# Performance work log

Measured on AMD Instinct MI355X. Metric: run time of the kernel, lower is better.

## Reference

```python
import jax, jax.numpy as jnp
import numpy as np

H, W = 256, 256
SIGMA = 1.5
INV_VAR = 1.0 / (2.0 * (SIGMA ** 2 + 1e-08))

def setup_inputs() -> dict:
    key = jax.random.key(0)
    k1, k2 = jax.random.split(key)
    B, K, N = 4, 8, 4096
    # pixel-coordinate points, slightly over-ranged to test edge behavior
    points_2d = jax.random.uniform(k1, (B, K, N, 2), dtype=jnp.float32,
                                   minval=-4.0, maxval=260.0)
    points_z = jax.random.uniform(k2, (B, K, N), dtype=jnp.float32,
                                  minval=0.0, maxval=5.0)
    return {"points_2d": points_2d, "points_z": points_z}

def reference(points_2d, points_z):
    # points_2d: (B, K, N, 2); points_z: (B, K, N)
    x = points_2d[..., 0]                      # (B,K,N)
    y = points_2d[..., 1]                      # (B,K,N)
    xg = jnp.arange(W, dtype=points_2d.dtype)  # (W,)
    yg = jnp.arange(H, dtype=points_2d.dtype)  # (H,)
    # Separable Gaussian: exp(-(dx^2+dy^2)*c) = exp(-dx^2*c) * exp(-dy^2*c)
    wx = jnp.exp(-((xg - x[..., None]) ** 2) * INV_VAR)  # (B,K,N,W)
    wy = jnp.exp(-((yg - y[..., None]) ** 2) * INV_VAR)  # (B,K,N,H)
    inv_z = 1.0 / jnp.clip(points_z, 1e-05, None)        # (B,K,N)
    wy = wy * inv_z[..., None]
    # sum over points of outer products -> (B,K,H,W)
    return jnp.einsum('bknh,bknw->bkhw', wy, wx)
```

## Files before the change

### kernel.cpp

```cpp
#include <hip/hip_runtime.h>
#include <hip/hip_bf16.h>

typedef __attribute__((ext_vector_type(8))) short bf16x8;
typedef __attribute__((ext_vector_type(4))) float f32x4;
typedef __attribute__((ext_vector_type(4))) unsigned int u32x4;

constexpr int NPTS = 4096;
constexpr int HH = 256;
constexpr int WW = 256;
constexpr int PSEG = 256;
constexpr int CCAPW = 288;

#define SCALE_S 0.56621453f
#define DCUT 10.0f

__device__ inline unsigned cvtpk(float lo, float hi) {
    unsigned r;
    asm("v_cvt_pk_bf16_f32 %0, %1, %2" : "=v"(r) : "v"(lo), "v"(hi));
    return r;
}

__global__ __launch_bounds__(256, 2) void soft_raster_kernel(
    const float* __restrict__ p2d,
    const float* __restrict__ pz,
    float* __restrict__ out)
{
    const int bk  = blockIdx.z;
    const int tm  = blockIdx.y * 64;
    const int tn  = blockIdx.x * 64;
    const int tid = threadIdx.x;

    __shared__ __align__(16) float sxs[4 * PSEG], sys[4 * PSEG], szi[4 * PSEG];
    __shared__ __align__(16) float cxs[4 * CCAPW], cys[4 * CCAPW], czi[4 * CCAPW];
    __shared__ int scnt[4];

    const int wid  = tid >> 6;
    const int lane = tid & 63;
    const int tmw  = tm + ((wid >> 1) << 5);
    const int tnw  = tn + ((wid & 1) << 5);
    const int g    = lane >> 4;
    const int r    = lane & 15;

    const size_t pbase = (size_t)bk * NPTS;
    const float4* __restrict__ pxy4 =
        reinterpret_cast<const float4*>(p2d + 2 * pbase);
    const float2* __restrict__ pz2 =
        reinterpret_cast<const float2*>(pz + pbase);

    const float Xlo = (float)tn - DCUT, Xhi = (float)(tn + 63) + DCUT;
    const float Ylo = (float)tm - DCUT, Yhi = (float)(tm + 63) + DCUT;
    const unsigned long long maskl = (1ull << lane) - 1ull;

    float4 P[8];
    float2 Z[8];
    #pragma unroll
    for (int it = 0; it < 8; ++it) P[it] = pxy4[(wid << 9) + (it << 6) + lane];
    #pragma unroll
    for (int it = 0; it < 8; ++it) Z[it] = pz2[(wid << 9) + (it << 6) + lane];

    int base = 0;
    #pragma unroll
    for (int it = 0; it < 8; ++it) {
        const float4 p  = P[it];
        const float2 zz = Z[it];
        bool in0 = (p.x > Xlo) && (p.x < Xhi) && (p.y > Ylo) && (p.y < Yhi);
        bool in1 = (p.z > Xlo) && (p.z < Xhi) && (p.w > Ylo) && (p.w < Yhi);
        unsigned long long be = __ballot(in0);
        unsigned long long bo = __ballot(in1);
        int pos0 = base + __popcll(be & maskl) + __popcll(bo & maskl);
        int pos1 = pos0 + (in0 ? 1 : 0);
        if (in0 && pos0 < PSEG) {
            const int s = (wid << 8) + pos0;
            sxs[s] = p.x * SCALE_S;
            sys[s] = p.y * SCALE_S;
            szi[s] = -__builtin_amdgcn_logf(fmaxf(zz.x, 1e-5f));
        }
        if (in1 && pos1 < PSEG) {
            const int s = (wid << 8) + pos1;
            sxs[s] = p.z * SCALE_S;
            sys[s] = p.w * SCALE_S;
            szi[s] = -__builtin_amdgcn_logf(fmaxf(zz.y, 1e-5f));
        }
        base += __popcll(be) + __popcll(bo);
    }
    if (lane == 0) scnt[wid] = (base < PSEG) ? base : PSEG;
    __syncthreads();

    const float xlo = ((float)tnw - DCUT) * SCALE_S;
    const float xhi = ((float)(tnw + 31) + DCUT) * SCALE_S;
    const float ylo = ((float)tmw - DCUT) * SCALE_S;
    const float yhi = ((float)(tmw + 31) + DCUT) * SCALE_S;
    float* __restrict__ wxs = cxs + wid * CCAPW;
    float* __restrict__ wys = cys + wid * CCAPW;
    float* __restrict__ wzi = czi + wid * CCAPW;

    int cw = 0;
    #pragma unroll
    for (int s = 0; s < 4; ++s) {
        const int cs = scnt[s];
        const int jb = lane << 2;
        const float4 x4 = *reinterpret_cast<const float4*>(&sxs[(s << 8) + jb]);
        const float4 y4 = *reinterpret_cast<const float4*>(&sys[(s << 8) + jb]);
        const float4 z4 = *reinterpret_cast<const float4*>(&szi[(s << 8) + jb]);
        bool i0 = (jb + 0 < cs) && (x4.x > xlo) && (x4.x < xhi) && (y4.x > ylo) && (y4.x < yhi);
        bool i1 = (jb + 1 < cs) && (x4.y > xlo) && (x4.y < xhi) && (y4.y > ylo) && (y4.y < yhi);
        bool i2 = (jb + 2 < cs) && (x4.z > xlo) && (x4.z < xhi) && (y4.z > ylo) && (y4.z < yhi);
        bool i3 = (jb + 3 < cs) && (x4.w > xlo) && (x4.w < xhi) && (y4.w > ylo) && (y4.w < yhi);
        unsigned long long b0 = __ballot(i0), b1 = __ballot(i1);
        unsigned long long b2 = __ballot(i2), b3 = __ballot(i3);
        const int c0 = __popcll(b0), c1 = __popcll(b1), c2 = __popcll(b2);
        int pos0 = cw + __popcll(b0 & maskl);
        int pos1 = cw + c0 + __popcll(b1 & maskl);
        int pos2 = cw + c0 + c1 + __popcll(b2 & maskl);
        int pos3 = cw + c0 + c1 + c2 + __popcll(b3 & maskl);
        if (i0 && pos0 < 256) { wxs[pos0] = x4.x; wys[pos0] = y4.x; wzi[pos0] = z4.x; }
        if (i1 && pos1 < 256) { wxs[pos1] = x4.y; wys[pos1] = y4.y; wzi[pos1] = z4.y; }
        if (i2 && pos2 < 256) { wxs[pos2] = x4.z; wys[pos2] = y4.z; wzi[pos2] = z4.z; }
        if (i3 && pos3 < 256) { wxs[pos3] = x4.w; wys[pos3] = y4.w; wzi[pos3] = z4.w; }
        cw += c0 + c1 + c2 + __popcll(b3);
    }
    cw = (cw < 256) ? cw : 256;
    const int pw = (cw + 31) & ~31;
    for (int j = cw + lane; j < pw; j += 64) {
        wxs[j] = 0.f; wys[j] = 0.f; wzi[j] = -__builtin_inff();
    }

    f32x4 acc[2][2] = {};
    const float qy0 = (float)(tmw + r)      * SCALE_S;
    const float qy1 = (float)(tmw + 16 + r) * SCALE_S;
    const float qx0 = (float)(tnw + r)      * SCALE_S;
    const float qx1 = (float)(tnw + 16 + r) * SCALE_S;

    for (int k0 = 0; k0 < pw; k0 += 32) {
        const int kb = k0 + (g << 3);

        float4 y0 = *reinterpret_cast<const float4*>(&wys[kb]);
        float4 y1 = *reinterpret_cast<const float4*>(&wys[kb + 4]);
        float4 z0 = *reinterpret_cast<const float4*>(&wzi[kb]);
        float4 z1 = *reinterpret_cast<const float4*>(&wzi[kb + 4]);
        float4 x0 = *reinterpret_cast<const float4*>(&wxs[kb]);
        float4 x1 = *reinterpret_cast<const float4*>(&wxs[kb + 4]);

        u32x4 au[2], bu[2];
        #pragma unroll
        for (int mi = 0; mi < 2; ++mi) {
            const float qy = mi ? qy1 : qy0;
            float d;
            d = qy - y0.x; const float a0 = __builtin_amdgcn_exp2f(fmaf(d, -d, z0.x));
            d = qy - y0.y; const float a1 = __builtin_amdgcn_exp2f(fmaf(d, -d, z0.y));
            d = qy - y0.z; const float a2 = __builtin_amdgcn_exp2f(fmaf(d, -d, z0.z));
            d = qy - y0.w; const float a3 = __builtin_amdgcn_exp2f(fmaf(d, -d, z0.w));
            d = qy - y1.x; const float a4 = __builtin_amdgcn_exp2f(fmaf(d, -d, z1.x));
            d = qy - y1.y; const float a5 = __builtin_amdgcn_exp2f(fmaf(d, -d, z1.y));
            d = qy - y1.z; const float a6 = __builtin_amdgcn_exp2f(fmaf(d, -d, z1.z));
            d = qy - y1.w; const float a7 = __builtin_amdgcn_exp2f(fmaf(d, -d, z1.w));
            au[mi][0] = cvtpk(a0, a1); au[mi][1] = cvtpk(a2, a3);
            au[mi][2] = cvtpk(a4, a5); au[mi][3] = cvtpk(a6, a7);
        }
        #pragma unroll
        for (int ni = 0; ni < 2; ++ni) {
            const float qx = ni ? qx1 : qx0;
            float d;
            d = qx - x0.x; const float b0 = __builtin_amdgcn_exp2f(-(d * d));
            d = qx - x0.y; const float b1 = __builtin_amdgcn_exp2f(-(d * d));
            d = qx - x0.z; const float b2 = __builtin_amdgcn_exp2f(-(d * d));
            d = qx - x0.w; const float b3 = __builtin_amdgcn_exp2f(-(d * d));
            d = qx - x1.x; const float b4 = __builtin_amdgcn_exp2f(-(d * d));
            d = qx - x1.y; const float b5 = __builtin_amdgcn_exp2f(-(d * d));
            d = qx - x1.z; const float b6 = __builtin_amdgcn_exp2f(-(d * d));
            d = qx - x1.w; const float b7 = __builtin_amdgcn_exp2f(-(d * d));
            bu[ni][0] = cvtpk(b0, b1); bu[ni][1] = cvtpk(b2, b3);
            bu[ni][2] = cvtpk(b4, b5); bu[ni][3] = cvtpk(b6, b7);
        }
        #pragma unroll
        for (int mi = 0; mi < 2; ++mi)
            #pragma unroll
            for (int ni = 0; ni < 2; ++ni)
                acc[mi][ni] = __builtin_amdgcn_mfma_f32_16x16x32_bf16(
                    __builtin_bit_cast(bf16x8, au[mi]),
                    __builtin_bit_cast(bf16x8, bu[ni]), acc[mi][ni], 0, 0, 0);
    }

    float* obase = out + (size_t)bk * (HH * WW);
    #pragma unroll
    for (int mi = 0; mi < 2; ++mi) {
        #pragma unroll
        for (int ni = 0; ni < 2; ++ni) {
            const int col  = tnw + (ni << 4) + r;
            const int row0 = tmw + (mi << 4) + (g << 2);
            #pragma unroll
            for (int j = 0; j < 4; ++j)
                obase[(size_t)(row0 + j) * WW + col] = acc[mi][ni][j];
        }
    }
}

extern "C" void kernel_launch(void* const* d_in, const int* in_sizes, int n_in,
                              void* d_out, int out_size, void* d_ws, size_t ws_size,
                              hipStream_t stream) {
    const float* p2d = (const float*)d_in[0];
    const float* pz  = (const float*)d_in[1];
    float* out       = (float*)d_out;
    const int nbk    = in_sizes[1] / NPTS;
    dim3 grid(WW / 64, HH / 64, nbk);
    dim3 block(256);
    hipLaunchKernelGGL(soft_raster_kernel, grid, block, 0, stream, p2d, pz, out);
}
```

Baseline: 15.07 us.

## Use 8 waves per block with 16x32 per-wave tiles and smaller candidate caps

Doubles the block to 512 threads (8 waves). Each wave now owns a 16x32 output sub-tile instead of 32x32, and the point-binning load is split across more waves with half the loads per thread. Per-wave candidate lists are capped at 192 points with a tighter y-bounds filter. This is meant to raise parallelism and latency hiding in the exp/MFMA loop. In exchange, the x-direction Gaussian weights are recomputed by twice as many waves, more LDS is used per block, and the lower cap could drop points in dense regions.

After: 17.89 us. +18.7%, slower.

```diff
diff --git a/kernel.cpp b/kernel.cpp
--- a/kernel.cpp
+++ b/kernel.cpp
@@ -8,8 +8,9 @@
 constexpr int NPTS = 4096;
 constexpr int HH = 256;
 constexpr int WW = 256;
-constexpr int PSEG = 256;
-constexpr int CCAPW = 288;
+constexpr int PSEG  = 256;
+constexpr int CWCAP = 192;
+constexpr int CCAPW = 224;
 
 #define SCALE_S 0.56621453f
 #define DCUT 10.0f
@@ -20,7 +21,7 @@
     return r;
 }
 
-__global__ __launch_bounds__(256, 2) void soft_raster_kernel(
+__global__ __launch_bounds__(512, 4) void soft_raster_kernel(
     const float* __restrict__ p2d,
     const float* __restrict__ pz,
     float* __restrict__ out)
@@ -30,13 +31,13 @@
     const int tn  = blockIdx.x * 64;
     const int tid = threadIdx.x;
 
-    __shared__ __align__(16) float sxs[4 * PSEG], sys[4 * PSEG], szi[4 * PSEG];
-    __shared__ __align__(16) float cxs[4 * CCAPW], cys[4 * CCAPW], czi[4 * CCAPW];
-    __shared__ int scnt[4];
+    __shared__ __align__(16) float sxs[8 * PSEG], sys[8 * PSEG], szi[8 * PSEG];
+    __shared__ __align__(16) float cxs[8 * CCAPW], cys[8 * CCAPW], czi[8 * CCAPW];
+    __shared__ int scnt[8];
 
     const int wid  = tid >> 6;
     const int lane = tid & 63;
-    const int tmw  = tm + ((wid >> 1) << 5);
+    const int tmw  = tm + ((wid >> 1) << 4);
     const int tnw  = tn + ((wid & 1) << 5);
     const int g    = lane >> 4;
     const int r    = lane & 15;
@@ -47,87 +48,99 @@
     const float2* __restrict__ pz2 =
         reinterpret_cast<const float2*>(pz + pbase);
 
+    const unsigned long long maskl = (1ull << lane) - 1ull;
+
     const float Xlo = (float)tn - DCUT, Xhi = (float)(tn + 63) + DCUT;
     const float Ylo = (float)tm - DCUT, Yhi = (float)(tm + 63) + DCUT;
-    const unsigned long long maskl = (1ull << lane) - 1ull;
-
-    float4 P[8];
-    float2 Z[8];
-    #pragma unroll
-    for (int it = 0; it < 8; ++it) P[it] = pxy4[(wid << 9) + (it << 6) + lane];
-    #pragma unroll
-    for (int it = 0; it < 8; ++it) Z[it] = pz2[(wid << 9) + (it << 6) + lane];
+
+    float4 P[4];
+    float2 Z[4];
+    #pragma unroll
+    for (int it = 0; it < 4; ++it) P[it] = pxy4[(wid << 8) + (it << 6) + lane];
+    #pragma unroll
+    for (int it = 0; it < 4; ++it) Z[it] = pz2[(wid << 8) + (it << 6) + lane];
+
+#define PSTEP(flag, xv, yv, zv)                                               \
+    {                                                                         \
+        unsigned long long b_ = __ballot(flag);                               \
+        int p_ = base + __popcll(b_ & maskl);                                 \
+        if ((flag) && p_ < PSEG) {                                            \
+            const int s_ = (wid << 8) + p_;                                   \
+            sxs[s_] = (xv) * SCALE_S;                                         \
+            sys[s_] = (yv) * SCALE_S;                                         \
+            szi[s_] = -__builtin_amdgcn_logf(fmaxf((zv), 1e-5f));             \
+        }                                                                     \
+        base += __popcll(b_);                                                 \
+    }
 
     int base = 0;
     #pragma unroll
-    for (int it = 0; it < 8; ++it) {
+    for (int it = 0; it < 4; ++it) {
         const float4 p  = P[it];
         const float2 zz = Z[it];
         bool in0 = (p.x > Xlo) && (p.x < Xhi) && (p.y > Ylo) && (p.y < Yhi);
         bool in1 = (p.z > Xlo) && (p.z < Xhi) && (p.w > Ylo) && (p.w < Yhi);
-        unsigned long long be = __ballot(in0);
-        unsigned long long bo = __ballot(in1);
-        int pos0 = base + __popcll(be & maskl) + __popcll(bo & maskl);
-        int pos1 = pos0 + (in0 ? 1 : 0);
-        if (in0 && pos0 < PSEG) {
-            const int s = (wid << 8) + pos0;
-            sxs[s] = p.x * SCALE_S;
-            sys[s] = p.y * SCALE_S;
-            szi[s] = -__builtin_amdgcn_logf(fmaxf(zz.x, 1e-5f));
-        }
-        if (in1 && pos1 < PSEG) {
-            const int s = (wid << 8) + pos1;
-            sxs[s] = p.z * SCALE_S;
-            sys[s] = p.w * SCALE_S;
-            szi[s] = -__builtin_amdgcn_logf(fmaxf(zz.y, 1e-5f));
-        }
-        base += __popcll(be) + __popcll(bo);
-    }
+        PSTEP(in0, p.x, p.y, zz.x);
+        PSTEP(in1, p.z, p.w, zz.y);
+    }
+#undef PSTEP
     if (lane == 0) scnt[wid] = (base < PSEG) ? base : PSEG;
     __syncthreads();
 
     const float xlo = ((float)tnw - DCUT) * SCALE_S;
     const float xhi = ((float)(tnw + 31) + DCUT) * SCALE_S;
     const float ylo = ((float)tmw - DCUT) * SCALE_S;
-    const float yhi = ((float)(tmw + 31) + DCUT) * SCALE_S;
+    const float yhi = ((float)(tmw + 15) + DCUT) * SCALE_S;
     float* __restrict__ wxs = cxs + wid * CCAPW;
     float* __restrict__ wys = cys + wid * CCAPW;
     float* __restrict__ wzi = czi + wid * CCAPW;
 
+#define FSTEP(flag, xv, yv, zv)                                               \
+    {                                                                         \
+        unsigned long long b_ = __ballot(flag);                               \
+        int p_ = cw + __popcll(b_ & maskl);                                   \
+        if ((flag) && p_ < CWCAP) { wxs[p_] = (xv); wys[p_] = (yv); wzi[p_] = (zv); } \
+        cw += __popcll(b_);                                                   \
+    }
+
     int cw = 0;
-    #pragma unroll
-    for (int s = 0; s < 4; ++s) {
-        const int cs = scnt[s];
-        const int jb = lane << 2;
-        const float4 x4 = *reinterpret_cast<const float4*>(&sxs[(s << 8) + jb]);
-        const float4 y4 = *reinterpret_cast<const float4*>(&sys[(s << 8) + jb]);
-        const float4 z4 = *reinterpret_cast<const float4*>(&szi[(s << 8) + jb]);
-        bool i0 = (jb + 0 < cs) && (x4.x > xlo) && (x4.x < xhi) && (y4.x > ylo) && (y4.x < yhi);
-        bool i1 = (jb + 1 < cs) && (x4.y > xlo) && (x4.y < xhi) && (y4.y > ylo) && (y4.y < yhi);
-        bool i2 = (jb + 2 < cs) && (x4.z > xlo) && (x4.z < xhi) && (y4.z > ylo) && (y4.z < yhi);
-        bool i3 = (jb + 3 < cs) && (x4.w > xlo) && (x4.w < xhi) && (y4.w > ylo) && (y4.w < yhi);
-        unsigned long long b0 = __ballot(i0), b1 = __ballot(i1);
-        unsigned long long b2 = __ballot(i2), b3 = __ballot(i3);
-        const int c0 = __popcll(b0), c1 = __popcll(b1), c2 = __popcll(b2);
-        int pos0 = cw + __popcll(b0 & maskl);
-        int pos1 = cw + c0 + __popcll(b1 & maskl);
-        int pos2 = cw + c0 + c1 + __popcll(b2 & maskl);
-        int pos3 = cw + c0 + c1 + c2 + __popcll(b3 & maskl);
-        if (i0 && pos0 < 256) { wxs[pos0] = x4.x; wys[pos0] = y4.x; wzi[pos0] = z4.x; }
-        if (i1 && pos1 < 256) { wxs[pos1] = x4.y; wys[pos1] = y4.y; wzi[pos1] = z4.y; }
-        if (i2 && pos2 < 256) { wxs[pos2] = x4.z; wys[pos2] = y4.z; wzi[pos2] = z4.z; }
-        if (i3 && pos3 < 256) { wxs[pos3] = x4.w; wys[pos3] = y4.w; wzi[pos3] = z4.w; }
-        cw += c0 + c1 + c2 + __popcll(b3);
-    }
-    cw = (cw < 256) ? cw : 256;
+    const int jb = lane << 2;
+    #pragma unroll
+    for (int s2 = 0; s2 < 4; ++s2) {
+        const int sa = s2 << 1, sb = sa | 1;
+        const int csa = scnt[sa], csb = scnt[sb];
+        const float4 xa = *reinterpret_cast<const float4*>(&sxs[(sa << 8) + jb]);
+        const float4 ya = *reinterpret_cast<const float4*>(&sys[(sa << 8) + jb]);
+        const float4 za = *reinterpret_cast<const float4*>(&szi[(sa << 8) + jb]);
+        const float4 xb = *reinterpret_cast<const float4*>(&sxs[(sb << 8) + jb]);
+        const float4 yb = *reinterpret_cast<const float4*>(&sys[(sb << 8) + jb]);
+        const float4 zb = *reinterpret_cast<const float4*>(&szi[(sb << 8) + jb]);
+        bool a0 = (jb + 0 < csa) && (xa.x > xlo) && (xa.x < xhi) && (ya.x > ylo) && (ya.x < yhi);
+        bool a1 = (jb + 1 < csa) && (xa.y > xlo) && (xa.y < xhi) && (ya.y > ylo) && (ya.y < yhi);
+        bool a2 = (jb + 2 < csa) && (xa.z > xlo) && (xa.z < xhi) && (ya.z > ylo) && (ya.z < yhi);
+        bool a3 = (jb + 3 < csa) && (xa.w > xlo) && (xa.w < xhi) && (ya.w > ylo) && (ya.w < yhi);
+        bool b0 = (jb + 0 < csb) && (xb.x > xlo) && (xb.x < xhi) && (yb.x > ylo) && (yb.x < yhi);
+        bool b1 = (jb + 1 < csb) && (xb.y > xlo) && (xb.y < xhi) && (yb.y > ylo) && (yb.y < yhi);
+        bool b2 = (jb + 2 < csb) && (xb.z > xlo) && (xb.z < xhi) && (yb.z > ylo) && (yb.z < yhi);
+        bool b3 = (jb + 3 < csb) && (xb.w > xlo) && (xb.w < xhi) && (yb.w > ylo) && (yb.w < yhi);
+        FSTEP(a0, xa.x, ya.x, za.x);
+        FSTEP(a1, xa.y, ya.y, za.y);
+        FSTEP(a2, xa.z, ya.z, za.z);
+        FSTEP(a3, xa.w, ya.w, za.w);
+        FSTEP(b0, xb.x, yb.x, zb.x);
+        FSTEP(b1, xb.y, yb.y, zb.y);
+        FSTEP(b2, xb.z, yb.z, zb.z);
+        FSTEP(b3, xb.w, yb.w, zb.w);
+    }
+#undef FSTEP
+    cw = (cw < CWCAP) ? cw : CWCAP;
     const int pw = (cw + 31) & ~31;
     for (int j = cw + lane; j < pw; j += 64) {
         wxs[j] = 0.f; wys[j] = 0.f; wzi[j] = -__builtin_inff();
     }
 
-    f32x4 acc[2][2] = {};
-    const float qy0 = (float)(tmw + r)      * SCALE_S;
-    const float qy1 = (float)(tmw + 16 + r) * SCALE_S;
+    f32x4 acc[2] = {};
+    const float qy  = (float)(tmw + r)      * SCALE_S;
     const float qx0 = (float)(tnw + r)      * SCALE_S;
     const float qx1 = (float)(tnw + 16 + r) * SCALE_S;
 
@@ -141,10 +154,8 @@
         float4 x0 = *reinterpret_cast<const float4*>(&wxs[kb]);
         float4 x1 = *reinterpret_cast<const float4*>(&wxs[kb + 4]);
 
-        u32x4 au[2], bu[2];
-        #pragma unroll
-        for (int mi = 0; mi < 2; ++mi) {
-            const float qy = mi ? qy1 : qy0;
+        u32x4 au, bu[2];
+        {
             float d;
             d = qy - y0.x; const float a0 = __builtin_amdgcn_exp2f(fmaf(d, -d, z0.x));
             d = qy - y0.y; const float a1 = __builtin_amdgcn_exp2f(fmaf(d, -d, z0.y));
@@ -154,8 +165,8 @@
             d = qy - y1.y; const float a5 = __builtin_amdgcn_exp2f(fmaf(d, -d, z1.y));
             d = qy - y1.z; const float a6 = __builtin_amdgcn_exp2f(fmaf(d, -d, z1.z));
             d = qy - y1.w; const float a7 = __builtin_amdgcn_exp2f(fmaf(d, -d, z1.w));
-            au[mi][0] = cvtpk(a0, a1); au[mi][1] = cvtpk(a2, a3);
-            au[mi][2] = cvtpk(a4, a5); au[mi][3] = cvtpk(a6, a7);
+            au[0] = cvtpk(a0, a1); au[1] = cvtpk(a2, a3);
+            au[2] = cvtpk(a4, a5); au[3] = cvtpk(a6, a7);
         }
         #pragma unroll
         for (int ni = 0; ni < 2; ++ni) {
@@ -173,25 +184,20 @@
             bu[ni][2] = cvtpk(b4, b5); bu[ni][3] = cvtpk(b6, b7);
         }
         #pragma unroll
-        for (int mi = 0; mi < 2; ++mi)
-            #pragma unroll
-            for (int ni = 0; ni < 2; ++ni)
-                acc[mi][ni] = __builtin_amdgcn_mfma_f32_16x16x32_bf16(
-                    __builtin_bit_cast(bf16x8, au[mi]),
-                    __builtin_bit_cast(bf16x8, bu[ni]), acc[mi][ni], 0, 0, 0);
+        for (int ni = 0; ni < 2; ++ni)
+            acc[ni] = __builtin_amdgcn_mfma_f32_16x16x32_bf16(
+                __builtin_bit_cast(bf16x8, au),
+                __builtin_bit_cast(bf16x8, bu[ni]), acc[ni], 0, 0, 0);
     }
 
     float* obase = out + (size_t)bk * (HH * WW);
-    #pragma unroll
-    for (int mi = 0; mi < 2; ++mi) {
+    const int row0 = tmw + (g << 2);
+    #pragma unroll
+    for (int ni = 0; ni < 2; ++ni) {
+        const int col = tnw + (ni << 4) + r;
         #pragma unroll
-        for (int ni = 0; ni < 2; ++ni) {
-            const int col  = tnw + (ni << 4) + r;
-            const int row0 = tmw + (mi << 4) + (g << 2);
-            #pragma unroll
-            for (int j = 0; j < 4; ++j)
-                obase[(size_t)(row0 + j) * WW + col] = acc[mi][ni][j];
-        }
+        for (int j = 0; j < 4; ++j)
+            obase[(size_t)(row0 + j) * WW + col] = acc[ni][j];
     }
 }
 
@@ -203,6 +209,6 @@
     float* out       = (float*)d_out;
     const int nbk    = in_sizes[1] / NPTS;
     dim3 grid(WW / 64, HH / 64, nbk);
-    dim3 block(256);
+    dim3 block(512);
     hipLaunchKernelGGL(soft_raster_kernel, grid, block, 0, stream, p2d, pz, out);
 }
```
